# Kernel tuning notes

Measured on AMD Instinct MI355X. Metric: run time of the kernel, lower is better.

The kernel has to match this reference:

```python
import jax, jax.numpy as jnp
import numpy as np
from jax import lax

B, KLEN, KDIM, QDIM, ADIM, VDIM = 32, 2000, 512, 512, 512, 512
CONV_CH, CONV_K = 10, 201

def setup_inputs() -> dict:
    key = jax.random.key(0)
    ks = jax.random.split(key, 16)
    s = lambda fan: 1.0 / np.sqrt(fan)
    return {
        "key": jax.random.normal(ks[0], (B, KLEN, KDIM), jnp.float32),
        "value": jax.random.normal(ks[1], (B, KLEN, VDIM), jnp.float32),
        "query": jax.random.normal(ks[2], (B, 1, QDIM), jnp.float32),
        "aw_prev": jnp.zeros((B, 1, KLEN), jnp.float32),
        "mask": jnp.ones((B, 1, KLEN), jnp.int32),
        # parameters (torch nn.Linear: y = x @ W.T + b, W is [out,in])
        "Wk": jax.random.uniform(ks[3], (ADIM, KDIM), jnp.float32, -s(KDIM), s(KDIM)),
        "bk": jax.random.uniform(ks[4], (ADIM,), jnp.float32, -s(KDIM), s(KDIM)),
        "Wq": jax.random.uniform(ks[5], (ADIM, QDIM), jnp.float32, -s(QDIM), s(QDIM)),
        "conv_w": jax.random.uniform(ks[6], (CONV_CH, 1, CONV_K), jnp.float32, -s(CONV_K), s(CONV_K)),
        "Wconv": jax.random.uniform(ks[7], (ADIM, CONV_CH), jnp.float32, -s(CONV_CH), s(CONV_CH)),
        "v": jax.random.uniform(ks[8], (ADIM,), jnp.float32, -s(ADIM), s(ADIM)),
    }

def reference(key, value, query, aw_prev, mask, Wk, bk, Wq, conv_w, Wconv, v):
    # location-aware attention, qlen == 1, sharpening_factor == 1, no dropout (eval)
    kproj = jnp.einsum('bkd,ad->bka', key, Wk) + bk              # [B, klen, adim]
    qproj = jnp.einsum('bqd,ad->bqa', query, Wq)                 # [B, 1, adim]
    # conv over previous attention weights: 1D 'same' conv, 1 -> CONV_CH channels
    conv_feat = lax.conv_general_dilated(
        aw_prev, conv_w, window_strides=(1,), padding='SAME',
        dimension_numbers=('NCH', 'OIH', 'NCH'))                 # [B, C, klen]
    conv_proj = jnp.einsum('bck,ac->bka', conv_feat, Wconv)      # [B, klen, adim]
    # additive score: v^T tanh(Wk k + Wq q + Wc f)
    tmp = jnp.tanh(kproj[:, None] + qproj[:, :, None] + conv_proj[:, None])  # [B,1,klen,adim]
    e = jnp.einsum('bqka,a->bqk', tmp, v)                        # [B, 1, klen]
    neg_inf = jnp.finfo(e.dtype).min
    e = jnp.where(mask == 0, neg_inf, e)
    aw = jax.nn.softmax(e, axis=-1)                              # [B, 1, klen]
    cv = jnp.einsum('bqk,bkv->bqv', aw, value)                   # [B, 1, vdim]
    return cv, aw[:, None]  # aw: [B, 1(H), 1(qlen), klen]
```

## Files before the change

kernel.cpp:

```cpp
#include <hip/hip_runtime.h>
#include <hip/hip_bf16.h>
#include <math.h>

#define B 32
#define KLEN 2000
#define KDIM 512
#define QDIM 512
#define ADIM 512
#define VDIM 512
#define CONV_CH 10
#define CONV_K 201
#define NROWS (B*KLEN)

#define NKS  33
#define ZERO16 {0,0,0,0,0,0,0,0,0,0,0,0,0,0,0,0}

#define NP_PACK 53
#define NP_QPRJ 26
#define NP_ZERO 26
#define NP_CONV 256

#define CH_LEN 63
#define CH_N   32

typedef __attribute__((ext_vector_type(8)))  short bf16x8;
typedef __attribute__((ext_vector_type(16))) float f32x16;
typedef __attribute__((ext_vector_type(4)))  float f32x4;
typedef __attribute__((ext_vector_type(2)))  float f32x2;

__device__ __forceinline__ ushort f32_to_bf16(float f) {
    union { float f; unsigned int u; } v; v.f = f;
    unsigned int x = v.u;
    unsigned int r = (x + 0x7FFFu + ((x >> 16) & 1u)) >> 16;
    return (ushort)r;
}

__device__ __forceinline__ float fast_tanh(float x) {
    return 1.0f - 2.0f / (__expf(2.0f * x) + 1.0f);
}

#define MFMA32(a, bfr, c) __builtin_amdgcn_mfma_f32_32x32x16_bf16(a, bfr, c, 0, 0, 0)

__global__ __launch_bounds__(640, 2)
void k_prep(const float* __restrict__ Wk, const float* __restrict__ Wconv,
            const float* __restrict__ bk, ushort* __restrict__ wp,
            const float* __restrict__ query, const float* __restrict__ Wq,
            float* __restrict__ qproj,
            const float* __restrict__ aw_prev, const float* __restrict__ conv_w,
            float* __restrict__ cf, float* __restrict__ cv) {
    __shared__ float w_s[CONV_CH * 204];
    __shared__ float aw_s[464];
    const int bid = blockIdx.x, tid = threadIdx.x;

    if (bid < NP_PACK) {
        int t = bid * 640 + tid;
        if (t < 16 * NKS * 64) {
            int lane = t & 63;
            int idx = t >> 6;
            int ks = idx % NKS, nt = idx / NKS;
            int h = lane >> 5, r = lane & 31;
            int a = nt * 32 + r;
            int j0 = ks * 16 + h * 8;
            union { uint4 v; ushort u[8]; } pk;
            #pragma unroll
            for (int jj = 0; jj < 8; jj++) {
                int j = j0 + jj;
                float val;
                if (j < 512)       val = Wk[a * KDIM + j];
                else if (j < 522)  val = Wconv[a * CONV_CH + (j - 512)];
                else if (j == 522) val = bk[a];
                else               val = 0.f;
                pk.u[jj] = f32_to_bf16(val);
            }
            *(uint4*)(wp + (size_t)t * 8) = pk.v;
        }
    } else if (bid < NP_PACK + NP_QPRJ) {
        int t = (bid - NP_PACK) * 640 + tid;
        if (t < B * ADIM) {
            int b = t >> 9, a = t & 511;
            const f32x4* q = (const f32x4*)(query + b * QDIM);
            const f32x4* w = (const f32x4*)(Wq + a * QDIM);
            float acc = 0.f;
            #pragma unroll 4
            for (int i = 0; i < 128; i++) {
                f32x4 qv = q[i], wv = w[i];
                acc += qv[0]*wv[0] + qv[1]*wv[1] + qv[2]*wv[2] + qv[3]*wv[3];
            }
            qproj[t] = acc;
        }
    } else if (bid < NP_PACK + NP_QPRJ + NP_ZERO) {
        int t = (bid - NP_PACK - NP_QPRJ) * 640 + tid;
        if (t < B * VDIM) cv[t] = 0.f;
    } else {
        int cb = bid - NP_PACK - NP_QPRJ - NP_ZERO;
        int b = cb >> 3, chunk = cb & 7;
        int k0 = chunk * 256;
        for (int i = tid; i < CONV_CH * 204; i += 640) {
            int c = i / 204, t = i % 204;
            w_s[i] = (t < CONV_K) ? conv_w[c * CONV_K + t] : 0.f;
        }
        for (int i = tid; i < 464; i += 640) {
            int src = k0 - 100 + i;
            aw_s[i] = (src >= 0 && src < KLEN) ? aw_prev[b * KLEN + src] : 0.f;
        }
        __syncthreads();

        const int c = tid >> 6;
        const int k_local = (tid & 63) * 4;
        const float* wc = w_s + c * 204;
        float a0 = 0.f, a1 = 0.f, a2 = 0.f, a3 = 0.f;
        f32x4 r0 = *(const f32x4*)(aw_s + k_local);
        #pragma unroll 3
        for (int q = 0; q < 51; q++) {
            f32x4 r1 = *(const f32x4*)(aw_s + k_local + 4 * q + 4);
            float w0 = wc[4*q], w1 = wc[4*q+1], w2 = wc[4*q+2], w3 = wc[4*q+3];
            a0 += w0*r0[0]; a1 += w0*r0[1]; a2 += w0*r0[2]; a3 += w0*r0[3];
            a0 += w1*r0[1]; a1 += w1*r0[2]; a2 += w1*r0[3]; a3 += w1*r1[0];
            a0 += w2*r0[2]; a1 += w2*r0[3]; a2 += w2*r1[0]; a3 += w2*r1[1];
            a0 += w3*r0[3]; a1 += w3*r1[0]; a2 += w3*r1[1]; a3 += w3*r1[2];
            r0 = r1;
        }
        int k = k0 + k_local;
        float* dst = cf + ((size_t)b * CONV_CH + c) * KLEN + k;
        if (k + 3 < KLEN) {
            f32x4 o; o[0] = a0; o[1] = a1; o[2] = a2; o[3] = a3;
            *(f32x4*)dst = o;
        } else {
            if (k     < KLEN) dst[0] = a0;
            if (k + 1 < KLEN) dst[1] = a1;
            if (k + 2 < KLEN) dst[2] = a2;
            if (k + 3 < KLEN) dst[3] = a3;
        }
    }
}

__global__ __launch_bounds__(512, 4)
void k_main(const float* __restrict__ key, const ushort* __restrict__ wp,
            const float* __restrict__ qproj, const float* __restrict__ cf,
            const float* __restrict__ vvec, const int* __restrict__ mask,
            float* __restrict__ e_out) {
    __shared__ char Alds[65536];
    __shared__ float partsum[8][2][32];
    const int tid = threadIdx.x;
    const int wc = tid >> 6, lane = tid & 63;
    const int r = lane & 31, h = lane >> 5;
    const int b = blockIdx.x >> 5;
    const int kbase = (blockIdx.x & 31) * 64;

    #pragma unroll
    for (int i = 0; i < 8; i++) {
        int ch = tid + i * 512;
        int arow = ch >> 6, cx = ch & 63;
        int kpos = kbase + arow; if (kpos >= KLEN) kpos = KLEN - 1;
        const float* kp = key + ((size_t)b * KLEN + kpos) * KDIM + cx * 8;
        f32x4 f0 = __builtin_nontemporal_load((const f32x4*)kp);
        f32x4 f1 = __builtin_nontemporal_load((const f32x4*)(kp + 4));
        union { uint4 v; ushort u[8]; } pk;
        pk.u[0] = f32_to_bf16(f0[0]); pk.u[1] = f32_to_bf16(f0[1]);
        pk.u[2] = f32_to_bf16(f0[2]); pk.u[3] = f32_to_bf16(f0[3]);
        pk.u[4] = f32_to_bf16(f1[0]); pk.u[5] = f32_to_bf16(f1[1]);
        pk.u[6] = f32_to_bf16(f1[2]); pk.u[7] = f32_to_bf16(f1[3]);
        int off = arow * 1024 + cx * 16;
        off ^= (arow & 31) << 4;
        *(uint4*)(Alds + off) = pk.v;
    }
    __syncthreads();

    const ushort* bpW0 = wp + ((size_t)(wc * 2 + 0) * NKS * 64 + lane) * 8;
    const ushort* bpW1 = wp + ((size_t)(wc * 2 + 1) * NKS * 64 + lane) * 8;
    const int base_g0 = r * 1024 + h * 16;
    const int base_g1 = base_g0 + 32768;
    const int swz = r << 4;

    f32x16 c00 = ZERO16, c01 = ZERO16;
    f32x16 c10 = ZERO16, c11 = ZERO16;

    #pragma unroll 4
    for (int ks = 0; ks < 32; ks++) {
        bf16x8 k0 = *(const bf16x8*)(Alds + ((base_g0 + ks * 32) ^ swz));
        bf16x8 k1 = *(const bf16x8*)(Alds + ((base_g1 + ks * 32) ^ swz));
        bf16x8 w0 = *(const bf16x8*)(bpW0 + ks * 512);
        bf16x8 w1 = *(const bf16x8*)(bpW1 + ks * 512);
        c00 = MFMA32(w0, k0, c00); c01 = MFMA32(w0, k1, c01);
        c10 = MFMA32(w1, k0, c10); c11 = MFMA32(w1, k1, c11);
    }
    {
        auto build_ext = [&](int kpos) -> bf16x8 {
            int kc = kpos < KLEN ? kpos : KLEN - 1;
            const float* cfb = cf + ((size_t)b * CONV_CH) * KLEN + kc;
            union { bf16x8 v8; ushort u[8]; } pk;
            if (h == 0) {
                #pragma unroll
                for (int jj = 0; jj < 8; jj++) pk.u[jj] = f32_to_bf16(cfb[(size_t)jj * KLEN]);
            } else {
                pk.u[0] = f32_to_bf16(cfb[(size_t)8 * KLEN]);
                pk.u[1] = f32_to_bf16(cfb[(size_t)9 * KLEN]);
                pk.u[2] = 0x3F80;
                pk.u[3] = 0; pk.u[4] = 0; pk.u[5] = 0; pk.u[6] = 0; pk.u[7] = 0;
            }
            return pk.v8;
        };
        bf16x8 x0 = build_ext(kbase + r);
        bf16x8 x1 = build_ext(kbase + 32 + r);
        bf16x8 w0 = *(const bf16x8*)(bpW0 + 32 * 512);
        bf16x8 w1 = *(const bf16x8*)(bpW1 + 32 * 512);
        c00 = MFMA32(w0, x0, c00); c01 = MFMA32(w0, x1, c01);
        c10 = MFMA32(w1, x0, c10); c11 = MFMA32(w1, x1, c11);
    }

    const float* qb = qproj + b * ADIM + wc * 64;
    const float* vb = vvec + wc * 64;
    float pg0 = 0.f, pg1 = 0.f;
    #pragma unroll
    for (int t = 0; t < 2; t++) {
        const f32x16 a0 = t ? c10 : c00;
        const f32x16 a1 = t ? c11 : c01;
        #pragma unroll
        for (int q = 0; q < 4; q++) {
            f32x4 qv = *(const f32x4*)(qb + t * 32 + 8 * q + 4 * h);
            f32x4 vv = *(const f32x4*)(vb + t * 32 + 8 * q + 4 * h);
            #pragma unroll
            for (int j = 0; j < 4; j++) {
                int i = 4 * q + j;
                pg0 += fast_tanh(a0[i] + qv[j]) * vv[j];
                pg1 += fast_tanh(a1[i] + qv[j]) * vv[j];
            }
        }
    }
    pg0 += __shfl_xor(pg0, 32);
    pg1 += __shfl_xor(pg1, 32);
    if (h == 0) { partsum[wc][0][r] = pg0; partsum[wc][1][r] = pg1; }
    __syncthreads();

    if (tid < 64) {
        int g = tid >> 5, rr = tid & 31;
        float s = 0.f;
        #pragma unroll
        for (int w = 0; w < 8; w++) s += partsum[w][g][rr];
        int kpos = kbase + g * 32 + rr;
        if (kpos < KLEN) {
            int idx = b * KLEN + kpos;
            e_out[idx] = mask[idx] ? s : -3.4028235e38f;
        }
    }
}

__global__ void k_stats(const float* __restrict__ e, float* __restrict__ stats) {
    int b = blockIdx.x;
    const float* er = e + b * KLEN;
    __shared__ float redm[4], reds[4];
    int tid = threadIdx.x, lane = tid & 63, wv = tid >> 6;
    float m = -3.4028235e38f;
    for (int k = tid; k < KLEN; k += 256) m = fmaxf(m, er[k]);
    for (int o = 32; o; o >>= 1) m = fmaxf(m, __shfl_xor(m, o));
    if (lane == 0) redm[wv] = m;
    __syncthreads();
    m = fmaxf(fmaxf(redm[0], redm[1]), fmaxf(redm[2], redm[3]));
    float s = 0.f;
    for (int k = tid; k < KLEN; k += 256) s += __expf(er[k] - m);
    for (int o = 32; o; o >>= 1) s += __shfl_xor(s, o);
    if (lane == 0) reds[wv] = s;
    __syncthreads();
    if (tid == 0) {
        s = reds[0] + reds[1] + reds[2] + reds[3];
        stats[b * 2] = m;
        stats[b * 2 + 1] = 1.0f / s;
    }
}

__global__ __launch_bounds__(512, 4)
void k_cvpart(const float* __restrict__ e, const float* __restrict__ stats,
              const float* __restrict__ value, float* __restrict__ aw,
              float* __restrict__ cv) {
    int b = blockIdx.x >> 5, chunk = blockIdx.x & 31;
    int k0 = chunk * CH_LEN;
    int len = KLEN - k0; if (len > CH_LEN) len = CH_LEN;
    __shared__ float sa[CH_LEN + 1];
    __shared__ f32x4 red[3][128];
    int tid = threadIdx.x;
    if (tid < len) {
        float m = stats[b * 2], inv = stats[b * 2 + 1];
        float p = __expf(e[b * KLEN + k0 + tid] - m) * inv;
        sa[tid] = p;
        aw[b * KLEN + k0 + tid] = p;
    }
    __syncthreads();
    const int kh = tid >> 7;
    const int colt = tid & 127;
    const float* vp = value + ((size_t)b * KLEN + k0) * VDIM + colt * 4;
    f32x4 acc = {0.f, 0.f, 0.f, 0.f};
    for (int k = kh; k < len; k += 4) {
        f32x4 vv = *(const f32x4*)(vp + (size_t)k * VDIM);
        acc += vv * sa[k];
    }
    if (kh) red[kh - 1][colt] = acc;
    __syncthreads();
    if (kh == 0) {
        acc += red[0][colt] + red[1][colt] + red[2][colt];
        float* dst = cv + b * VDIM + colt * 4;
        atomicAdd(dst + 0, acc[0]);
        atomicAdd(dst + 1, acc[1]);
        atomicAdd(dst + 2, acc[2]);
        atomicAdd(dst + 3, acc[3]);
    }
}

extern "C" void kernel_launch(void* const* d_in, const int* in_sizes, int n_in,
                              void* d_out, int out_size, void* d_ws, size_t ws_size,
                              hipStream_t stream) {
    const float* key     = (const float*)d_in[0];
    const float* value   = (const float*)d_in[1];
    const float* query   = (const float*)d_in[2];
    const float* aw_prev = (const float*)d_in[3];
    const int*   mask    = (const int*)d_in[4];
    const float* Wk      = (const float*)d_in[5];
    const float* bk      = (const float*)d_in[6];
    const float* Wq      = (const float*)d_in[7];
    const float* conv_w  = (const float*)d_in[8];
    const float* Wconv   = (const float*)d_in[9];
    const float* vvec    = (const float*)d_in[10];

    char* ws = (char*)d_ws;
    ushort* wp   = (ushort*)(ws + 0);
    float* qproj = (float*)(ws + 540672);
    float* cf    = (float*)(ws + 606208);
    float* e     = (float*)(ws + 3166208);
    float* stats = (float*)(ws + 3422208);

    float* cv = (float*)d_out;
    float* aw = (float*)d_out + B * VDIM;

    k_prep  <<<NP_PACK + NP_QPRJ + NP_ZERO + NP_CONV, 640, 0, stream>>>(
                Wk, Wconv, bk, wp, query, Wq, qproj, aw_prev, conv_w, cf, cv);
    k_main  <<<1024, 512, 0, stream>>>(key, wp, qproj, cf, vvec, mask, e);
    k_stats <<<B,    256, 0, stream>>>(e, stats);
    k_cvpart<<<B*32, 512, 0, stream>>>(e, stats, value, aw, cv);
}
```

Before: 141.8 us.

## Fuse softmax stats into cv kernel and use packed bf16 conversion

Removes the separate k_stats launch. Each of the 32 chunk blocks per batch now recomputes the row max and sum over 2000 scores before computing its slice of aw and the context vector. This drops one kernel launch and the dependency gap before it, at the cost of redundant reductions, since every row of e is read 32 times. It also replaces the manual scalar fp32-to-bf16 rounding in k_main's key pack and conv-feature pack with the paired __float22bfloat162_rn conversion, which may map to a packed conversion instruction.

```diff
diff --git a/kernel.cpp b/kernel.cpp
--- a/kernel.cpp
+++ b/kernel.cpp
@@ -21,18 +21,23 @@
 #define NP_CONV 256
 
 #define CH_LEN 63
-#define CH_N   32
 
 typedef __attribute__((ext_vector_type(8)))  short bf16x8;
 typedef __attribute__((ext_vector_type(16))) float f32x16;
 typedef __attribute__((ext_vector_type(4)))  float f32x4;
-typedef __attribute__((ext_vector_type(2)))  float f32x2;
 
 __device__ __forceinline__ ushort f32_to_bf16(float f) {
     union { float f; unsigned int u; } v; v.f = f;
     unsigned int x = v.u;
     unsigned int r = (x + 0x7FFFu + ((x >> 16) & 1u)) >> 16;
     return (ushort)r;
+}
+
+__device__ __forceinline__ unsigned int pk_bf16(float lo, float hi) {
+    union { __hip_bfloat162 h2; unsigned int u; } c;
+    float2 t; t.x = lo; t.y = hi;
+    c.h2 = __float22bfloat162_rn(t);
+    return c.u;
 }
 
 __device__ __forceinline__ float fast_tanh(float x) {
@@ -155,14 +160,14 @@
         const float* kp = key + ((size_t)b * KLEN + kpos) * KDIM + cx * 8;
         f32x4 f0 = __builtin_nontemporal_load((const f32x4*)kp);
         f32x4 f1 = __builtin_nontemporal_load((const f32x4*)(kp + 4));
-        union { uint4 v; ushort u[8]; } pk;
-        pk.u[0] = f32_to_bf16(f0[0]); pk.u[1] = f32_to_bf16(f0[1]);
-        pk.u[2] = f32_to_bf16(f0[2]); pk.u[3] = f32_to_bf16(f0[3]);
-        pk.u[4] = f32_to_bf16(f1[0]); pk.u[5] = f32_to_bf16(f1[1]);
-        pk.u[6] = f32_to_bf16(f1[2]); pk.u[7] = f32_to_bf16(f1[3]);
-        int off = arow * 1024 + cx * 16;
+        uint4 pk;
+        pk.x = pk_bf16(f0[0], f0[1]);
+        pk.y = pk_bf16(f0[2], f0[3]);
+        pk.z = pk_bf16(f1[0], f1[1]);
+        pk.w = pk_bf16(f1[2], f1[3]);
+        int off = (arow << 10) + (cx << 4);
         off ^= (arow & 31) << 4;
-        *(uint4*)(Alds + off) = pk.v;
+        *(uint4*)(Alds + off) = pk;
     }
     __syncthreads();
 
@@ -188,15 +193,17 @@
         auto build_ext = [&](int kpos) -> bf16x8 {
             int kc = kpos < KLEN ? kpos : KLEN - 1;
             const float* cfb = cf + ((size_t)b * CONV_CH) * KLEN + kc;
-            union { bf16x8 v8; ushort u[8]; } pk;
+            union { bf16x8 v8; unsigned int u[4]; ushort us[8]; } pk;
             if (h == 0) {
-                #pragma unroll
-                for (int jj = 0; jj < 8; jj++) pk.u[jj] = f32_to_bf16(cfb[(size_t)jj * KLEN]);
+                pk.u[0] = pk_bf16(cfb[0],              cfb[(size_t)1 * KLEN]);
+                pk.u[1] = pk_bf16(cfb[(size_t)2*KLEN], cfb[(size_t)3 * KLEN]);
+                pk.u[2] = pk_bf16(cfb[(size_t)4*KLEN], cfb[(size_t)5 * KLEN]);
+                pk.u[3] = pk_bf16(cfb[(size_t)6*KLEN], cfb[(size_t)7 * KLEN]);
             } else {
-                pk.u[0] = f32_to_bf16(cfb[(size_t)8 * KLEN]);
-                pk.u[1] = f32_to_bf16(cfb[(size_t)9 * KLEN]);
-                pk.u[2] = 0x3F80;
-                pk.u[3] = 0; pk.u[4] = 0; pk.u[5] = 0; pk.u[6] = 0; pk.u[7] = 0;
+                pk.u[0] = pk_bf16(cfb[(size_t)8*KLEN], cfb[(size_t)9 * KLEN]);
+                pk.us[2] = 0x3F80;
+                pk.us[3] = 0;
+                pk.u[2] = 0; pk.u[3] = 0;
             }
             return pk.v8;
         };
@@ -245,46 +252,41 @@
     }
 }
 
-__global__ void k_stats(const float* __restrict__ e, float* __restrict__ stats) {
-    int b = blockIdx.x;
+__global__ __launch_bounds__(512, 4)
+void k_cv(const float* __restrict__ e, const float* __restrict__ value,
+          float* __restrict__ aw, float* __restrict__ cv) {
+    int b = blockIdx.x >> 5, chunk = blockIdx.x & 31;
     const float* er = e + b * KLEN;
-    __shared__ float redm[4], reds[4];
+    __shared__ float redv[8];
+    __shared__ float sa[CH_LEN + 1];
+    __shared__ f32x4 red[3][128];
     int tid = threadIdx.x, lane = tid & 63, wv = tid >> 6;
+
     float m = -3.4028235e38f;
-    for (int k = tid; k < KLEN; k += 256) m = fmaxf(m, er[k]);
+    for (int k = tid; k < KLEN; k += 512) m = fmaxf(m, er[k]);
     for (int o = 32; o; o >>= 1) m = fmaxf(m, __shfl_xor(m, o));
-    if (lane == 0) redm[wv] = m;
-    __syncthreads();
-    m = fmaxf(fmaxf(redm[0], redm[1]), fmaxf(redm[2], redm[3]));
+    if (lane == 0) redv[wv] = m;
+    __syncthreads();
+    m = fmaxf(fmaxf(fmaxf(redv[0], redv[1]), fmaxf(redv[2], redv[3])),
+              fmaxf(fmaxf(redv[4], redv[5]), fmaxf(redv[6], redv[7])));
+    __syncthreads();
     float s = 0.f;
-    for (int k = tid; k < KLEN; k += 256) s += __expf(er[k] - m);
+    for (int k = tid; k < KLEN; k += 512) s += __expf(er[k] - m);
     for (int o = 32; o; o >>= 1) s += __shfl_xor(s, o);
-    if (lane == 0) reds[wv] = s;
-    __syncthreads();
-    if (tid == 0) {
-        s = reds[0] + reds[1] + reds[2] + reds[3];
-        stats[b * 2] = m;
-        stats[b * 2 + 1] = 1.0f / s;
-    }
-}
-
-__global__ __launch_bounds__(512, 4)
-void k_cvpart(const float* __restrict__ e, const float* __restrict__ stats,
-              const float* __restrict__ value, float* __restrict__ aw,
-              float* __restrict__ cv) {
-    int b = blockIdx.x >> 5, chunk = blockIdx.x & 31;
+    if (lane == 0) redv[wv] = s;
+    __syncthreads();
+    s = redv[0] + redv[1] + redv[2] + redv[3] + redv[4] + redv[5] + redv[6] + redv[7];
+    const float inv = 1.0f / s;
+
     int k0 = chunk * CH_LEN;
     int len = KLEN - k0; if (len > CH_LEN) len = CH_LEN;
-    __shared__ float sa[CH_LEN + 1];
-    __shared__ f32x4 red[3][128];
-    int tid = threadIdx.x;
     if (tid < len) {
-        float m = stats[b * 2], inv = stats[b * 2 + 1];
-        float p = __expf(e[b * KLEN + k0 + tid] - m) * inv;
+        float p = __expf(er[k0 + tid] - m) * inv;
         sa[tid] = p;
         aw[b * KLEN + k0 + tid] = p;
     }
     __syncthreads();
+
     const int kh = tid >> 7;
     const int colt = tid & 127;
     const float* vp = value + ((size_t)b * KLEN + k0) * VDIM + colt * 4;
@@ -325,14 +327,12 @@
     float* qproj = (float*)(ws + 540672);
     float* cf    = (float*)(ws + 606208);
     float* e     = (float*)(ws + 3166208);
-    float* stats = (float*)(ws + 3422208);
 
     float* cv = (float*)d_out;
     float* aw = (float*)d_out + B * VDIM;
 
-    k_prep  <<<NP_PACK + NP_QPRJ + NP_ZERO + NP_CONV, 640, 0, stream>>>(
-                Wk, Wconv, bk, wp, query, Wq, qproj, aw_prev, conv_w, cf, cv);
-    k_main  <<<1024, 512, 0, stream>>>(key, wp, qproj, cf, vvec, mask, e);
-    k_stats <<<B,    256, 0, stream>>>(e, stats);
-    k_cvpart<<<B*32, 512, 0, stream>>>(e, stats, value, aw, cv);
-}
+    k_prep<<<NP_PACK + NP_QPRJ + NP_ZERO + NP_CONV, 640, 0, stream>>>(
+              Wk, Wconv, bk, wp, query, Wq, qproj, aw_prev, conv_w, cf, cv);
+    k_main<<<1024, 512, 0, stream>>>(key, wp, qproj, cf, vvec, mask, e);
+    k_cv  <<<B*32, 512, 0, stream>>>(e, value, aw, cv);
+}
```

Result: no change. 140.2 us, median of 2 (-1.1%).
